# Kernel tuning notes

Measured on AMD Instinct MI355X. Metric: run time of the kernel, lower is better.

The kernel has to match this reference:

```python
import jax, jax.numpy as jnp
import numpy as np

INPUT_SIZE = (224, 224)


def setup_inputs() -> dict:
    key = jax.random.key(0)
    k1, k2, k3 = jax.random.split(key, 3)
    feat2 = jax.random.normal(k1, (16, 512, 28, 28), dtype=jnp.float32)
    feat3 = jax.random.normal(k2, (16, 1024, 14, 14), dtype=jnp.float32)
    memory_bank = jax.random.normal(k3, (16384, 1536), dtype=jnp.float32)
    return {"feat2": feat2, "feat3": feat3, "memory_bank": memory_bank}


def reference(feat2, feat3, memory_bank):
    b, c2, h, w = feat2.shape
    c3 = feat3.shape[1]
    # interpolate(feat3, size=(h,w), mode='bilinear', align_corners=False)
    feat3_up = jax.image.resize(feat3, (b, c3, h, w), method='bilinear')
    features = jnp.concatenate([feat2, feat3_up], axis=1)  # [b, c, h, w]
    c = c2 + c3
    feats = features.transpose(0, 2, 3, 1).reshape(-1, c)  # [N, c]
    x_sq = jnp.sum(feats * feats, axis=1, keepdims=True)            # [N, 1]
    m_sq = jnp.sum(memory_bank * memory_bank, axis=1)[None, :]      # [1, M]
    d2 = x_sq + m_sq - 2.0 * (feats @ memory_bank.T)                # [N, M]
    min_d = jnp.sqrt(jnp.maximum(jnp.min(d2, axis=1), 0.0))         # [N]
    anomaly_map = min_d.reshape(b, 1, h, w)
    anomaly_map = jax.image.resize(
        anomaly_map, (b, 1, INPUT_SIZE[0], INPUT_SIZE[1]), method='bilinear')
    pred_score = jnp.max(anomaly_map.reshape(b, -1), axis=1)
    return anomaly_map, pred_score
```

## Files before the change

### kernel.cpp

```cpp
#include <hip/hip_runtime.h>
#include <math.h>

#define N_ROWS 12544
#define C_DIM  1536
#define M_ROWS 16384
#define BATCH  16

#define QS    16.0f
#define S2x2  0.0078125f
#define S2    0.00390625f

typedef int   i32x4 __attribute__((ext_vector_type(4)));
typedef unsigned char u8;
typedef signed char   i8;

__device__ __forceinline__ unsigned fkey(float f) {
  unsigned u = __float_as_uint(f);
  return (u & 0x80000000u) ? ~u : (u | 0x80000000u);
}
__device__ __forceinline__ float funkey(unsigned k) {
  unsigned u = (k & 0x80000000u) ? (k ^ 0x80000000u) : ~k;
  return __uint_as_float(u);
}

__device__ __forceinline__ void gl_lds16(const void* g, void* l) {
  __builtin_amdgcn_global_load_lds(
      (__attribute__((address_space(1))) void*)(g),
      (__attribute__((address_space(3))) void*)(l), 16, 0, 0);
}

__device__ __forceinline__ int quant(float v) {
  int q = __float2int_rn(v * QS);
  return max(-127, min(127, q));
}

#define FSTRIDE 1552

__global__ __launch_bounds__(512) void prep_all(
    const float* __restrict__ feat2, const float* __restrict__ feat3,
    const float* __restrict__ mb,
    i8* __restrict__ feats, i8* __restrict__ mbb,
    float* __restrict__ xsq, float* __restrict__ msq,
    unsigned* __restrict__ dmin, unsigned* __restrict__ score) {
  const int blk = blockIdx.x;
  const int t = threadIdx.x;
  __shared__ u8 fsm[28 * FSTRIDE];
  __shared__ int sxq[28];

  if (blk >= 448) {
    const int wave = t >> 6, lane = t & 63;
    const int row = (blk - 448) * 8 + wave;
    const float* in = mb + (size_t)row * C_DIM;
    i8* outp = mbb + (size_t)row * C_DIM;
    float ssq = 0.f;
#pragma unroll
    for (int i = 0; i < 6; i++) {
      const int f4 = lane + 64 * i;
      const float4 v = *(const float4*)(in + f4 * 4);
      int q0 = quant(v.x), q1 = quant(v.y), q2 = quant(v.z), q3 = quant(v.w);
      unsigned w = (unsigned)(q0 & 0xFF) | ((unsigned)(q1 & 0xFF) << 8)
                 | ((unsigned)(q2 & 0xFF) << 16) | ((unsigned)(q3 & 0xFF) << 24);
      *(unsigned*)(outp + f4 * 4) = w;
      ssq += (float)(q0*q0 + q1*q1 + q2*q2 + q3*q3);
    }
    for (int off = 32; off > 0; off >>= 1) ssq += __shfl_down(ssq, off, 64);
    if (lane == 0) msq[row] = S2 * ssq;
  } else {
    const int b = blk / 28, y = blk % 28;
    const int n0 = b * 784 + y * 28;

    const float sy = 0.5f * y - 0.25f;
    const int y0 = (int)floorf(sy); const float fy = sy - (float)y0;
    const int y0c = max(y0, 0), y1c = min(y0 + 1, 13);
    const float wy0 = 1.f - fy, wy1 = fy;

    const int g  = t >> 5;
    const int l2 = t & 31;
    const float sx = 0.5f * l2 - 0.25f;
    const int x0 = (int)floorf(sx); const float fx = sx - (float)x0;
    const int x0c = max(x0, 0), x1c = min(x0 + 1, 13);
    const float wx0 = 1.f - fx, wx1 = fx;

    if (t < 28) sxq[t] = 0;

    const float* f2b = feat2 + (size_t)b * 512 * 784 + y * 28;
#pragma unroll 4
    for (int i = 0; i < 32; i++) {
      const int c = i * 16 + g;
      if (l2 < 28) {
        float v = f2b[(size_t)c * 784 + l2];
        fsm[l2 * FSTRIDE + c] = (u8)(i8)quant(v);
      }
    }

    const float* f3b = feat3 + (size_t)b * 1024 * 196;
#pragma unroll 4
    for (int i = 0; i < 64; i++) {
      const int cc = i * 16 + g;
      const float* f3 = f3b + (size_t)cc * 196;
      float v = 0.f;
      if (l2 < 14)       v = f3[y0c * 14 + l2];
      else if (l2 < 28)  v = f3[y1c * 14 + (l2 - 14)];
      float t0 = wy0 * __shfl(v, x0c, 32)      + wy1 * __shfl(v, 14 + x0c, 32);
      float t1 = wy0 * __shfl(v, x1c, 32)      + wy1 * __shfl(v, 14 + x1c, 32);
      if (l2 < 28) {
        float o = wx0 * t0 + wx1 * t1;
        fsm[l2 * FSTRIDE + 512 + cc] = (u8)(i8)quant(o);
      }
    }
    __syncthreads();

    i8* orow = feats + (size_t)n0 * C_DIM;
    for (int idx = t; idx < 28 * 96; idx += 512) {
      const int row = idx / 96, col = idx % 96;
      i32x4 wv = *(const i32x4*)(fsm + row * FSTRIDE + col * 16);
      *(i32x4*)(orow + (size_t)row * C_DIM + col * 16) = wv;
      int s = 0;
#pragma unroll
      for (int k = 0; k < 4; k++) {
        const int w = wv[k];
        const int b0 = (int)(i8)(w & 0xFF), b1 = (int)(i8)((w >> 8) & 0xFF);
        const int b2 = (int)(i8)((w >> 16) & 0xFF), b3 = (int)(i8)(w >> 24);
        s += b0*b0 + b1*b1 + b2*b2 + b3*b3;
      }
      atomicAdd(&sxq[row], s);
    }
    __syncthreads();
    if (t < 28) {
      xsq[n0 + t] = S2 * (float)sxq[t];
      dmin[n0 + t] = 0xFFFFFFFFu;
    }
    if (blk == 0 && t < BATCH) score[t] = 0u;
  }
}

__global__ __launch_bounds__(256) void gemm_min(
    const i8* __restrict__ X, const i8* __restrict__ Mb,
    const float* __restrict__ msq, unsigned* __restrict__ dmin) {
  __shared__ u8 As[16384];
  __shared__ u8 Bs[16384];
  __shared__ unsigned smin[128];
  const int t = threadIdx.x;
  const int bid = blockIdx.x;
  const int xcd = bid & 7, per = bid >> 3;
  const int mtile = (xcd << 4) | (per & 15);
  const int ntile = per >> 4;
  const int lane = t & 63, wave = t >> 6;
  const int wm = wave >> 1, wn = wave & 1;
  if (t < 128) smin[t] = 0xFFFFFFFFu;

  const int row0 = ntile * 128;
  const int col0 = mtile * 128;
  const int s_row = t >> 2;
  const int s_ch  = (t & 3) ^ ((t >> 3) & 3);
  const i8* ga = X  + (size_t)(row0 + s_row) * C_DIM + s_ch * 16;
  const i8* gb = Mb + (size_t)(col0 + s_row) * C_DIM + s_ch * 16;
  u8* la = As + t * 16;
  u8* lb = Bs + t * 16;

  i32x4 acc[4][4];
  const i32x4 zero = {0, 0, 0, 0};
#pragma unroll
  for (int mi = 0; mi < 4; mi++)
#pragma unroll
    for (int ni = 0; ni < 4; ni++) acc[mi][ni] = zero;

  const int quad = lane >> 4, l16 = lane & 15;
  const int fsw = (l16 >> 1) & 3;
  const int slot = ((quad ^ fsw) * 16);
  const u8* arow = As + (wm * 64 + l16) * 64 + slot;
  const u8* brow = Bs + (wn * 64 + l16) * 64 + slot;

  for (int k0 = 0; k0 < C_DIM; k0 += 128) {
    __syncthreads();
    gl_lds16(ga + k0,                    la);
    gl_lds16(ga + 64 * C_DIM + k0,       la + 4096);
    gl_lds16(ga + k0 + 64,               la + 8192);
    gl_lds16(ga + 64 * C_DIM + k0 + 64,  la + 12288);
    gl_lds16(gb + k0,                    lb);
    gl_lds16(gb + 64 * C_DIM + k0,       lb + 4096);
    gl_lds16(gb + k0 + 64,               lb + 8192);
    gl_lds16(gb + 64 * C_DIM + k0 + 64,  lb + 12288);
    __syncthreads();
#pragma unroll
    for (int sub = 0; sub < 2; sub++) {
      i32x4 af[4], bf[4];
#pragma unroll
      for (int mi = 0; mi < 4; mi++)
        af[mi] = *(const i32x4*)(arow + sub * 8192 + mi * 1024);
#pragma unroll
      for (int ni = 0; ni < 4; ni++)
        bf[ni] = *(const i32x4*)(brow + sub * 8192 + ni * 1024);
#pragma unroll
      for (int mi = 0; mi < 4; mi++)
#pragma unroll
        for (int ni = 0; ni < 4; ni++)
          acc[mi][ni] = __builtin_amdgcn_mfma_i32_16x16x64_i8(
              af[mi], bf[ni], acc[mi][ni], 0, 0, 0);
    }
  }

  float msql[4];
#pragma unroll
  for (int ni = 0; ni < 4; ni++)
    msql[ni] = msq[col0 + wn * 64 + ni * 16 + l16];

#pragma unroll
  for (int mi = 0; mi < 4; mi++) {
#pragma unroll
    for (int r = 0; r < 4; r++) {
      float v = msql[0] - S2x2 * (float)acc[mi][0][r];
#pragma unroll
      for (int ni = 1; ni < 4; ni++)
        v = fminf(v, msql[ni] - S2x2 * (float)acc[mi][ni][r]);
      v = fminf(v, __shfl_xor(v, 1, 64));
      v = fminf(v, __shfl_xor(v, 2, 64));
      v = fminf(v, __shfl_xor(v, 4, 64));
      v = fminf(v, __shfl_xor(v, 8, 64));
      if (l16 == 0) {
        int lrow = wm * 64 + mi * 16 + quad * 4 + r;
        atomicMin(&smin[lrow], fkey(v));
      }
    }
  }
  __syncthreads();
  if (t < 128) atomicMin(&dmin[row0 + t], smin[t]);
}

__global__ void finalize(const unsigned* __restrict__ dmin,
                         const float* __restrict__ xsq,
                         float* __restrict__ out) {
  const int b = blockIdx.x, slice = blockIdx.y, t = threadIdx.x;
  __shared__ float smap[784];
  __shared__ float sred[4];
  for (int i = t; i < 784; i += 256) {
    float d2 = xsq[b * 784 + i] + funkey(dmin[b * 784 + i]);
    smap[i] = sqrtf(fmaxf(d2, 0.f));
  }
  __syncthreads();
  float* omap = out + (size_t)b * 50176;
  float tmax = 0.f;
  const int p0 = slice * 6272;
  for (int p = p0 + t; p < p0 + 6272; p += 256) {
    const int Y = p / 224, Xp = p % 224;
    const float sy = Y * 0.125f - 0.4375f;
    const float sx = Xp * 0.125f - 0.4375f;
    const int y0 = (int)floorf(sy); const float fy = sy - (float)y0;
    const int x0 = (int)floorf(sx); const float fx = sx - (float)x0;
    const int y0c = max(y0, 0), y1c = min(y0 + 1, 27);
    const int x0c = max(x0, 0), x1c = min(x0 + 1, 27);
    float v = (1.f-fy)*((1.f-fx)*smap[y0c*28+x0c] + fx*smap[y0c*28+x1c])
            +      fy *((1.f-fx)*smap[y1c*28+x0c] + fx*smap[y1c*28+x1c]);
    omap[p] = v;
    tmax = fmaxf(tmax, v);
  }
  for (int off = 32; off > 0; off >>= 1)
    tmax = fmaxf(tmax, __shfl_down(tmax, off, 64));
  if ((t & 63) == 0) sred[t >> 6] = tmax;
  __syncthreads();
  if (t == 0) {
    float m = fmaxf(fmaxf(sred[0], sred[1]), fmaxf(sred[2], sred[3]));
    atomicMax((unsigned*)(out + 802816 + b), __float_as_uint(m));
  }
}

extern "C" void kernel_launch(void* const* d_in, const int* in_sizes, int n_in,
                              void* d_out, int out_size, void* d_ws, size_t ws_size,
                              hipStream_t stream) {
  const float* feat2 = (const float*)d_in[0];
  const float* feat3 = (const float*)d_in[1];
  const float* mb    = (const float*)d_in[2];
  char* ws = (char*)d_ws;
  i8*       feats = (i8*)ws;
  i8*       mbb   = (i8*)(ws + 19267584);
  float*    xsq   = (float*)(ws + 44433408);
  float*    msq   = (float*)(ws + 44483584);
  unsigned* dmin  = (unsigned*)(ws + 44549120);
  float* out = (float*)d_out;

  prep_all<<<448 + 2048, 512, 0, stream>>>(
      feat2, feat3, mb, feats, mbb, xsq, msq, dmin,
      (unsigned*)(out + 802816));
  gemm_min<<<12544, 256, 0, stream>>>(feats, mbb, msq, dmin);
  finalize<<<dim3(BATCH, 8), 256, 0, stream>>>(dmin, xsq, out);
}
```

Baseline: 517.5 us.

## Double-buffer GEMM LDS tiles and split prep blocks into channel thirds

The int8 GEMM now uses two LDS buffers, so the global-to-LDS load of the next K tile is issued before the MFMA work on the current tile, hiding load latency and dropping one barrier per iteration. The prep kernel's feature blocks are split three ways by channel range (feat2, and two halves of upsampled feat3), giving more parallel blocks and smaller shared memory. Row squared norms are now accumulated with global integer atomics, and the initialisation moves to hipMemsetAsync calls. LDS use per GEMM block doubles, which may lower occupancy, and the extra memset launches add some overhead.

Result: slower. 567.8 us (+9.7%).

```diff
diff --git a/kernel.cpp b/kernel.cpp
--- a/kernel.cpp
+++ b/kernel.cpp
@@ -34,22 +34,21 @@
   return max(-127, min(127, q));
 }
 
-#define FSTRIDE 1552
+#define FSTRIDE 528
 
 __global__ __launch_bounds__(512) void prep_all(
     const float* __restrict__ feat2, const float* __restrict__ feat3,
     const float* __restrict__ mb,
     i8* __restrict__ feats, i8* __restrict__ mbb,
-    float* __restrict__ xsq, float* __restrict__ msq,
-    unsigned* __restrict__ dmin, unsigned* __restrict__ score) {
+    int* __restrict__ xsqi, float* __restrict__ msq) {
   const int blk = blockIdx.x;
   const int t = threadIdx.x;
   __shared__ u8 fsm[28 * FSTRIDE];
   __shared__ int sxq[28];
 
-  if (blk >= 448) {
+  if (blk >= 1344) {
     const int wave = t >> 6, lane = t & 63;
-    const int row = (blk - 448) * 8 + wave;
+    const int row = (blk - 1344) * 8 + wave;
     const float* in = mb + (size_t)row * C_DIM;
     i8* outp = mbb + (size_t)row * C_DIM;
     float ssq = 0.f;
@@ -66,7 +65,8 @@
     for (int off = 32; off > 0; off >>= 1) ssq += __shfl_down(ssq, off, 64);
     if (lane == 0) msq[row] = S2 * ssq;
   } else {
-    const int b = blk / 28, y = blk % 28;
+    const int half = blk % 3, p = blk / 3;
+    const int b = p / 28, y = p % 28;
     const int n0 = b * 784 + y * 28;
 
     const float sy = 0.5f * y - 0.25f;
@@ -83,36 +83,40 @@
 
     if (t < 28) sxq[t] = 0;
 
-    const float* f2b = feat2 + (size_t)b * 512 * 784 + y * 28;
+    if (half == 0) {
+      const float* f2b = feat2 + (size_t)b * 512 * 784 + y * 28;
 #pragma unroll 4
-    for (int i = 0; i < 32; i++) {
-      const int c = i * 16 + g;
-      if (l2 < 28) {
-        float v = f2b[(size_t)c * 784 + l2];
-        fsm[l2 * FSTRIDE + c] = (u8)(i8)quant(v);
+      for (int i = 0; i < 32; i++) {
+        const int c = i * 16 + g;
+        if (l2 < 28) {
+          float v = f2b[(size_t)c * 784 + l2];
+          fsm[l2 * FSTRIDE + c] = (u8)(i8)quant(v);
+        }
       }
-    }
-
-    const float* f3b = feat3 + (size_t)b * 1024 * 196;
+    } else {
+      const int cc0 = (half - 1) * 512;
+      const float* f3b = feat3 + (size_t)b * 1024 * 196;
 #pragma unroll 4
-    for (int i = 0; i < 64; i++) {
-      const int cc = i * 16 + g;
-      const float* f3 = f3b + (size_t)cc * 196;
-      float v = 0.f;
-      if (l2 < 14)       v = f3[y0c * 14 + l2];
-      else if (l2 < 28)  v = f3[y1c * 14 + (l2 - 14)];
-      float t0 = wy0 * __shfl(v, x0c, 32)      + wy1 * __shfl(v, 14 + x0c, 32);
-      float t1 = wy0 * __shfl(v, x1c, 32)      + wy1 * __shfl(v, 14 + x1c, 32);
-      if (l2 < 28) {
-        float o = wx0 * t0 + wx1 * t1;
-        fsm[l2 * FSTRIDE + 512 + cc] = (u8)(i8)quant(o);
+      for (int i = 0; i < 32; i++) {
+        const int cc = cc0 + i * 16 + g;
+        const float* f3 = f3b + (size_t)cc * 196;
+        float v = 0.f;
+        if (l2 < 14)       v = f3[y0c * 14 + l2];
+        else if (l2 < 28)  v = f3[y1c * 14 + (l2 - 14)];
+        float t0 = wy0 * __shfl(v, x0c, 32)     + wy1 * __shfl(v, 14 + x0c, 32);
+        float t1 = wy0 * __shfl(v, x1c, 32)     + wy1 * __shfl(v, 14 + x1c, 32);
+        if (l2 < 28) {
+          float o = wx0 * t0 + wx1 * t1;
+          fsm[l2 * FSTRIDE + (i * 16 + g)] = (u8)(i8)quant(o);
+        }
       }
     }
     __syncthreads();
 
-    i8* orow = feats + (size_t)n0 * C_DIM;
-    for (int idx = t; idx < 28 * 96; idx += 512) {
-      const int row = idx / 96, col = idx % 96;
+    const int c0 = half * 512;
+    i8* orow = feats + (size_t)n0 * C_DIM + c0;
+    for (int idx = t; idx < 28 * 32; idx += 512) {
+      const int row = idx / 32, col = idx % 32;
       i32x4 wv = *(const i32x4*)(fsm + row * FSTRIDE + col * 16);
       *(i32x4*)(orow + (size_t)row * C_DIM + col * 16) = wv;
       int s = 0;
@@ -126,19 +130,15 @@
       atomicAdd(&sxq[row], s);
     }
     __syncthreads();
-    if (t < 28) {
-      xsq[n0 + t] = S2 * (float)sxq[t];
-      dmin[n0 + t] = 0xFFFFFFFFu;
-    }
-    if (blk == 0 && t < BATCH) score[t] = 0u;
+    if (t < 28) atomicAdd(&xsqi[n0 + t], sxq[t]);
   }
 }
 
 __global__ __launch_bounds__(256) void gemm_min(
     const i8* __restrict__ X, const i8* __restrict__ Mb,
     const float* __restrict__ msq, unsigned* __restrict__ dmin) {
-  __shared__ u8 As[16384];
-  __shared__ u8 Bs[16384];
+  __shared__ u8 As[32768];
+  __shared__ u8 Bs[32768];
   __shared__ unsigned smin[128];
   const int t = threadIdx.x;
   const int bid = blockIdx.x;
@@ -171,34 +171,50 @@
   const u8* arow = As + (wm * 64 + l16) * 64 + slot;
   const u8* brow = Bs + (wn * 64 + l16) * 64 + slot;
 
-  for (int k0 = 0; k0 < C_DIM; k0 += 128) {
+#define STAGE(BUF, K0) { \
+    gl_lds16(ga + (K0),                    la + (BUF) * 16384); \
+    gl_lds16(ga + 64 * C_DIM + (K0),       la + (BUF) * 16384 + 4096); \
+    gl_lds16(ga + (K0) + 64,               la + (BUF) * 16384 + 8192); \
+    gl_lds16(ga + 64 * C_DIM + (K0) + 64,  la + (BUF) * 16384 + 12288); \
+    gl_lds16(gb + (K0),                    lb + (BUF) * 16384); \
+    gl_lds16(gb + 64 * C_DIM + (K0),       lb + (BUF) * 16384 + 4096); \
+    gl_lds16(gb + (K0) + 64,               lb + (BUF) * 16384 + 8192); \
+    gl_lds16(gb + 64 * C_DIM + (K0) + 64,  lb + (BUF) * 16384 + 12288); }
+
+#define COMPUTE(BUF) { \
+    _Pragma("unroll") \
+    for (int sub = 0; sub < 2; sub++) { \
+      i32x4 af[4], bf[4]; \
+      _Pragma("unroll") \
+      for (int mi = 0; mi < 4; mi++) \
+        af[mi] = *(const i32x4*)(arow + (BUF) * 16384 + sub * 8192 + mi * 1024); \
+      _Pragma("unroll") \
+      for (int ni = 0; ni < 4; ni++) \
+        bf[ni] = *(const i32x4*)(brow + (BUF) * 16384 + sub * 8192 + ni * 1024); \
+      _Pragma("unroll") \
+      for (int mi = 0; mi < 4; mi++) \
+        _Pragma("unroll") \
+        for (int ni = 0; ni < 4; ni++) \
+          acc[mi][ni] = __builtin_amdgcn_mfma_i32_16x16x64_i8( \
+              af[mi], bf[ni], acc[mi][ni], 0, 0, 0); } }
+
+  STAGE(0, 0);
+  __syncthreads();
+  for (int ks = 0; ks < 10; ks += 2) {
+    STAGE(1, (ks + 1) * 128);
+    COMPUTE(0);
     __syncthreads();
-    gl_lds16(ga + k0,                    la);
-    gl_lds16(ga + 64 * C_DIM + k0,       la + 4096);
-    gl_lds16(ga + k0 + 64,               la + 8192);
-    gl_lds16(ga + 64 * C_DIM + k0 + 64,  la + 12288);
-    gl_lds16(gb + k0,                    lb);
-    gl_lds16(gb + 64 * C_DIM + k0,       lb + 4096);
-    gl_lds16(gb + k0 + 64,               lb + 8192);
-    gl_lds16(gb + 64 * C_DIM + k0 + 64,  lb + 12288);
+    STAGE(0, (ks + 2) * 128);
+    COMPUTE(1);
     __syncthreads();
-#pragma unroll
-    for (int sub = 0; sub < 2; sub++) {
-      i32x4 af[4], bf[4];
-#pragma unroll
-      for (int mi = 0; mi < 4; mi++)
-        af[mi] = *(const i32x4*)(arow + sub * 8192 + mi * 1024);
-#pragma unroll
-      for (int ni = 0; ni < 4; ni++)
-        bf[ni] = *(const i32x4*)(brow + sub * 8192 + ni * 1024);
-#pragma unroll
-      for (int mi = 0; mi < 4; mi++)
-#pragma unroll
-        for (int ni = 0; ni < 4; ni++)
-          acc[mi][ni] = __builtin_amdgcn_mfma_i32_16x16x64_i8(
-              af[mi], bf[ni], acc[mi][ni], 0, 0, 0);
-    }
-  }
+  }
+  STAGE(1, 11 * 128);
+  COMPUTE(0);
+  __syncthreads();
+  COMPUTE(1);
+
+#undef COMPUTE
+#undef STAGE
 
   float msql[4];
 #pragma unroll
@@ -228,13 +244,13 @@
 }
 
 __global__ void finalize(const unsigned* __restrict__ dmin,
-                         const float* __restrict__ xsq,
+                         const int* __restrict__ xsqi,
                          float* __restrict__ out) {
   const int b = blockIdx.x, slice = blockIdx.y, t = threadIdx.x;
   __shared__ float smap[784];
   __shared__ float sred[4];
   for (int i = t; i < 784; i += 256) {
-    float d2 = xsq[b * 784 + i] + funkey(dmin[b * 784 + i]);
+    float d2 = S2 * (float)xsqi[b * 784 + i] + funkey(dmin[b * 784 + i]);
     smap[i] = sqrtf(fmaxf(d2, 0.f));
   }
   __syncthreads();
@@ -273,14 +289,16 @@
   char* ws = (char*)d_ws;
   i8*       feats = (i8*)ws;
   i8*       mbb   = (i8*)(ws + 19267584);
-  float*    xsq   = (float*)(ws + 44433408);
+  int*      xsqi  = (int*)(ws + 44433408);
   float*    msq   = (float*)(ws + 44483584);
   unsigned* dmin  = (unsigned*)(ws + 44549120);
   float* out = (float*)d_out;
 
-  prep_all<<<448 + 2048, 512, 0, stream>>>(
-      feat2, feat3, mb, feats, mbb, xsq, msq, dmin,
-      (unsigned*)(out + 802816));
+  hipMemsetAsync(xsqi, 0, N_ROWS * 4, stream);
+  hipMemsetAsync(dmin, 0xFF, N_ROWS * 4, stream);
+  hipMemsetAsync(out + 802816, 0, BATCH * 4, stream);
+  prep_all<<<1344 + 2048, 512, 0, stream>>>(
+      feat2, feat3, mb, feats, mbb, xsqi, msq);
   gemm_min<<<12544, 256, 0, stream>>>(feats, mbb, msq, dmin);
-  finalize<<<dim3(BATCH, 8), 256, 0, stream>>>(dmin, xsq, out);
-}
+  finalize<<<dim3(BATCH, 8), 256, 0, stream>>>(dmin, xsqi, out);
+}
```

## Split feature prep into three channel-slice blocks and switch gemm grid to 2D

Applied to the files above, without the earlier changes.

Each (batch,row) feature-prep block is split into three blocks, one per 512-channel slice (feat2, and two halves of the upsampled feat3). This triples the prep parallelism and shrinks shared memory per block. Per-row squared norms are now accumulated with integer global atomics, and the buffer initialisation moves to hipMemsetAsync calls. The GEMM grid becomes a 2D launch with a simpler XCD-aware tile mapping and no explicit launch bounds. The changes add atomics and extra memset launches, and the new tile ordering may alter cache reuse in the GEMM.

After: 512.8 us. About the same (-0.9%).

```diff
diff --git a/kernel.cpp b/kernel.cpp
--- a/kernel.cpp
+++ b/kernel.cpp
@@ -34,22 +34,21 @@
   return max(-127, min(127, q));
 }
 
-#define FSTRIDE 1552
+#define FSTRIDE 528
 
 __global__ __launch_bounds__(512) void prep_all(
     const float* __restrict__ feat2, const float* __restrict__ feat3,
     const float* __restrict__ mb,
     i8* __restrict__ feats, i8* __restrict__ mbb,
-    float* __restrict__ xsq, float* __restrict__ msq,
-    unsigned* __restrict__ dmin, unsigned* __restrict__ score) {
+    int* __restrict__ xsqi, float* __restrict__ msq) {
   const int blk = blockIdx.x;
   const int t = threadIdx.x;
   __shared__ u8 fsm[28 * FSTRIDE];
   __shared__ int sxq[28];
 
-  if (blk >= 448) {
+  if (blk >= 1344) {
     const int wave = t >> 6, lane = t & 63;
-    const int row = (blk - 448) * 8 + wave;
+    const int row = (blk - 1344) * 8 + wave;
     const float* in = mb + (size_t)row * C_DIM;
     i8* outp = mbb + (size_t)row * C_DIM;
     float ssq = 0.f;
@@ -66,7 +65,8 @@
     for (int off = 32; off > 0; off >>= 1) ssq += __shfl_down(ssq, off, 64);
     if (lane == 0) msq[row] = S2 * ssq;
   } else {
-    const int b = blk / 28, y = blk % 28;
+    const int half = blk % 3, p = blk / 3;
+    const int b = p / 28, y = p % 28;
     const int n0 = b * 784 + y * 28;
 
     const float sy = 0.5f * y - 0.25f;
@@ -83,36 +83,40 @@
 
     if (t < 28) sxq[t] = 0;
 
-    const float* f2b = feat2 + (size_t)b * 512 * 784 + y * 28;
+    if (half == 0) {
+      const float* f2b = feat2 + (size_t)b * 512 * 784 + y * 28;
 #pragma unroll 4
-    for (int i = 0; i < 32; i++) {
-      const int c = i * 16 + g;
-      if (l2 < 28) {
-        float v = f2b[(size_t)c * 784 + l2];
-        fsm[l2 * FSTRIDE + c] = (u8)(i8)quant(v);
-      }
-    }
-
-    const float* f3b = feat3 + (size_t)b * 1024 * 196;
+      for (int i = 0; i < 32; i++) {
+        const int c = i * 16 + g;
+        if (l2 < 28) {
+          float v = f2b[(size_t)c * 784 + l2];
+          fsm[l2 * FSTRIDE + c] = (u8)(i8)quant(v);
+        }
+      }
+    } else {
+      const int cc0 = (half - 1) * 512;
+      const float* f3b = feat3 + (size_t)b * 1024 * 196;
 #pragma unroll 4
-    for (int i = 0; i < 64; i++) {
-      const int cc = i * 16 + g;
-      const float* f3 = f3b + (size_t)cc * 196;
-      float v = 0.f;
-      if (l2 < 14)       v = f3[y0c * 14 + l2];
-      else if (l2 < 28)  v = f3[y1c * 14 + (l2 - 14)];
-      float t0 = wy0 * __shfl(v, x0c, 32)      + wy1 * __shfl(v, 14 + x0c, 32);
-      float t1 = wy0 * __shfl(v, x1c, 32)      + wy1 * __shfl(v, 14 + x1c, 32);
-      if (l2 < 28) {
-        float o = wx0 * t0 + wx1 * t1;
-        fsm[l2 * FSTRIDE + 512 + cc] = (u8)(i8)quant(o);
-      }
-    }
-    __syncthreads();
-
-    i8* orow = feats + (size_t)n0 * C_DIM;
-    for (int idx = t; idx < 28 * 96; idx += 512) {
-      const int row = idx / 96, col = idx % 96;
+      for (int i = 0; i < 32; i++) {
+        const int cc = cc0 + i * 16 + g;
+        const float* f3 = f3b + (size_t)cc * 196;
+        float v = 0.f;
+        if (l2 < 14)       v = f3[y0c * 14 + l2];
+        else if (l2 < 28)  v = f3[y1c * 14 + (l2 - 14)];
+        float t0 = wy0 * __shfl(v, x0c, 32)     + wy1 * __shfl(v, 14 + x0c, 32);
+        float t1 = wy0 * __shfl(v, x1c, 32)     + wy1 * __shfl(v, 14 + x1c, 32);
+        if (l2 < 28) {
+          float o = wx0 * t0 + wx1 * t1;
+          fsm[l2 * FSTRIDE + (i * 16 + g)] = (u8)(i8)quant(o);
+        }
+      }
+    }
+    __syncthreads();
+
+    const int c0 = half * 512;
+    i8* orow = feats + (size_t)n0 * C_DIM + c0;
+    for (int idx = t; idx < 28 * 32; idx += 512) {
+      const int row = idx / 32, col = idx % 32;
       i32x4 wv = *(const i32x4*)(fsm + row * FSTRIDE + col * 16);
       *(i32x4*)(orow + (size_t)row * C_DIM + col * 16) = wv;
       int s = 0;
@@ -126,25 +130,20 @@
       atomicAdd(&sxq[row], s);
     }
     __syncthreads();
-    if (t < 28) {
-      xsq[n0 + t] = S2 * (float)sxq[t];
-      dmin[n0 + t] = 0xFFFFFFFFu;
-    }
-    if (blk == 0 && t < BATCH) score[t] = 0u;
-  }
-}
-
-__global__ __launch_bounds__(256) void gemm_min(
-    const i8* __restrict__ X, const i8* __restrict__ Mb,
-    const float* __restrict__ msq, unsigned* __restrict__ dmin) {
+    if (t < 28) atomicAdd(&xsqi[n0 + t], sxq[t]);
+  }
+}
+
+__global__ void gemm_min(const i8* __restrict__ X, const i8* __restrict__ Mb,
+                         const float* __restrict__ msq,
+                         unsigned* __restrict__ dmin) {
   __shared__ u8 As[16384];
   __shared__ u8 Bs[16384];
   __shared__ unsigned smin[128];
   const int t = threadIdx.x;
-  const int bid = blockIdx.x;
-  const int xcd = bid & 7, per = bid >> 3;
-  const int mtile = (xcd << 4) | (per & 15);
-  const int ntile = per >> 4;
+  const int bx = blockIdx.x;
+  const int mtile = ((bx & 7) << 4) | (bx >> 3);
+  const int ntile = blockIdx.y;
   const int lane = t & 63, wave = t >> 6;
   const int wm = wave >> 1, wn = wave & 1;
   if (t < 128) smin[t] = 0xFFFFFFFFu;
@@ -228,13 +227,13 @@
 }
 
 __global__ void finalize(const unsigned* __restrict__ dmin,
-                         const float* __restrict__ xsq,
+                         const int* __restrict__ xsqi,
                          float* __restrict__ out) {
   const int b = blockIdx.x, slice = blockIdx.y, t = threadIdx.x;
   __shared__ float smap[784];
   __shared__ float sred[4];
   for (int i = t; i < 784; i += 256) {
-    float d2 = xsq[b * 784 + i] + funkey(dmin[b * 784 + i]);
+    float d2 = S2 * (float)xsqi[b * 784 + i] + funkey(dmin[b * 784 + i]);
     smap[i] = sqrtf(fmaxf(d2, 0.f));
   }
   __syncthreads();
@@ -273,14 +272,16 @@
   char* ws = (char*)d_ws;
   i8*       feats = (i8*)ws;
   i8*       mbb   = (i8*)(ws + 19267584);
-  float*    xsq   = (float*)(ws + 44433408);
+  int*      xsqi  = (int*)(ws + 44433408);
   float*    msq   = (float*)(ws + 44483584);
   unsigned* dmin  = (unsigned*)(ws + 44549120);
   float* out = (float*)d_out;
 
-  prep_all<<<448 + 2048, 512, 0, stream>>>(
-      feat2, feat3, mb, feats, mbb, xsq, msq, dmin,
-      (unsigned*)(out + 802816));
-  gemm_min<<<12544, 256, 0, stream>>>(feats, mbb, msq, dmin);
-  finalize<<<dim3(BATCH, 8), 256, 0, stream>>>(dmin, xsq, out);
-}
+  hipMemsetAsync(xsqi, 0, N_ROWS * 4, stream);
+  hipMemsetAsync(dmin, 0xFF, N_ROWS * 4, stream);
+  hipMemsetAsync(out + 802816, 0, BATCH * 4, stream);
+  prep_all<<<1344 + 2048, 512, 0, stream>>>(
+      feat2, feat3, mb, feats, mbb, xsqi, msq);
+  gemm_min<<<dim3(128, 98), 256, 0, stream>>>(feats, mbb, msq, dmin);
+  finalize<<<dim3(BATCH, 8), 256, 0, stream>>>(dmin, xsqi, out);
+}
```
